# Kernel tuning notes

Measured on AMD Instinct MI355X. Metric: run time of the kernel, lower is better.

The kernel has to match this reference:

```python
import jax, jax.numpy as jnp
import numpy as np

N = 50000   # num_nodes
T = 8       # num_time_steps
C = 64      # feature width (num_features == hidden == num_classes == 64, forced by the module's shape constraints)
E = 800000  # num_edges


def temporal_conv(x, edge_index, time_index, W, b, perturb=None):
    """Faithful TemporalAGNNConv.forward: per-timestep masked scatter-add of
    neighbor features, concat over T, linear + relu. Implemented as a single
    fused (t, dst)-bucketed segment reduce instead of T separate propagates.
    Note: self.lin is dead code in the original; self-loop addition in the
    original would crash (time_index length mismatch) so edges are used as-is.
    """
    src, dst = edge_index[0], edge_index[1]
    msgs = x[src]                                   # [E, C] gather
    seg = time_index * N + dst                      # combined (t, node) bucket
    agg = jax.ops.segment_sum(msgs, seg, num_segments=T * N)   # [T*N, C]
    cat = agg.reshape(T, N, C).transpose(1, 0, 2).reshape(N, T * C)  # [N, T*C]
    out = jax.nn.relu(cat @ W + b)                  # temporal_lin + relu
    if perturb is not None:
        out = out + perturb
    return out


def setup_inputs() -> dict:
    key = jax.random.key(0)
    ks = jax.random.split(key, 11)
    x = jax.random.normal(ks[0], (N, C), jnp.float32)
    edge_index = jax.random.randint(ks[1], (2, E), 0, N, dtype=jnp.int32)
    time_index = jax.random.randint(ks[2], (E,), 0, T, dtype=jnp.int32)
    s_t = 1.0 / np.sqrt(T * C).astype(np.float32)
    # temporal_lin weights stored as [in, out] (torch Linear transposed)
    Wt1 = jax.random.uniform(ks[3], (T * C, C), jnp.float32, -s_t, s_t)
    bt1 = jax.random.uniform(ks[4], (C,), jnp.float32, -s_t, s_t)
    Wt2 = jax.random.uniform(ks[5], (T * C, C), jnp.float32, -s_t, s_t)
    bt2 = jax.random.uniform(ks[6], (C,), jnp.float32, -s_t, s_t)
    s_a1 = 1.0 / np.sqrt(C).astype(np.float32)
    Wa1 = jax.random.uniform(ks[7], (C, 128), jnp.float32, -s_a1, s_a1)
    ba1 = jax.random.uniform(ks[8], (128,), jnp.float32, -s_a1, s_a1)
    s_a2 = 1.0 / np.sqrt(128).astype(np.float32)
    Wa2 = jax.random.uniform(ks[9], (128, C), jnp.float32, -s_a2, s_a2)
    ba2 = jax.random.uniform(ks[10], (C,), jnp.float32, -s_a2, s_a2)
    return {"x": x, "edge_index": edge_index, "time_index": time_index,
            "Wt1": Wt1, "bt1": bt1, "Wt2": Wt2, "bt2": bt2,
            "Wa1": Wa1, "ba1": ba1, "Wa2": Wa2, "ba2": ba2}


def reference(x, edge_index, time_index, Wt1, bt1, Wt2, bt2, Wa1, ba1, Wa2, ba2):
    h1 = jax.nn.relu(temporal_conv(x, edge_index, time_index, Wt1, bt1))   # conv1 + relu
    h2 = temporal_conv(h1, edge_index, time_index, Wt2, bt2)               # conv2 (output width C)
    adv = jax.nn.relu(h2 @ Wa1 + ba1) @ Wa2 + ba2                          # adversary MLP -> [N, C]
    out = temporal_conv(x, edge_index, time_index, Wt1, bt1, perturb=adv)  # conv1 again + perturbation
    return out
```

## Files before the change

### kernel.cpp

```cpp
#include <hip/hip_runtime.h>

#define N_NODES 50000
#define C_FEAT  64
#define E_EDGES 800000
#define KEYS    400000
#define NBLK1   391
#define DPB     16
#define PBLK_X  1563
#define PBLK_W  128
#define PBLK_A  64
#define PBLK_H  3128
#define DPART   6250

typedef __attribute__((ext_vector_type(8))) short short8;
typedef __attribute__((ext_vector_type(4))) float f32x4;

__device__ __forceinline__ float bf2f(unsigned short u) {
    union { unsigned int i; float f; } v; v.i = ((unsigned int)u) << 16; return v.f;
}
__device__ __forceinline__ unsigned short f2bf(float f) {
    union { float f; unsigned int i; } v; v.f = f;
    unsigned int r = v.i + 0x7fff + ((v.i >> 16) & 1);
    return (unsigned short)(r >> 16);
}

__global__ __launch_bounds__(256) void prep_hist(const float* __restrict__ x,
                                                 const float* __restrict__ W1,
                                                 const float* __restrict__ W2,
                                                 const float* __restrict__ Wa1,
                                                 const float* __restrict__ Wa2,
                                                 const int* __restrict__ dst,
                                                 const int* __restrict__ tix,
                                                 unsigned short* __restrict__ xb,
                                                 unsigned short* __restrict__ WT1,
                                                 unsigned short* __restrict__ WT2,
                                                 unsigned short* __restrict__ Wa1T,
                                                 unsigned short* __restrict__ Wa2T,
                                                 int* __restrict__ cnt) {
    const int b = blockIdx.x;
    if (b < PBLK_X) {
        int base = (b * 256 + threadIdx.x) * 8;
        if (base < N_NODES * 64) {
            float4 a = *(const float4*)(x + base);
            float4 c = *(const float4*)(x + base + 4);
            short8 o;
            o[0] = (short)f2bf(a.x); o[1] = (short)f2bf(a.y);
            o[2] = (short)f2bf(a.z); o[3] = (short)f2bf(a.w);
            o[4] = (short)f2bf(c.x); o[5] = (short)f2bf(c.y);
            o[6] = (short)f2bf(c.z); o[7] = (short)f2bf(c.w);
            *(short8*)(xb + base) = o;
        }
    } else if (b < PBLK_X + PBLK_W) {
        int i = (b - PBLK_X) * 256 + threadIdx.x;
        int n = i >> 9, k = i & 511;
        WT1[i] = f2bf(W1[k * 64 + n]);
        WT2[i] = f2bf(W2[k * 64 + n]);
    } else if (b < PBLK_X + PBLK_W + PBLK_A) {
        int i = (b - PBLK_X - PBLK_W) * 256 + threadIdx.x;
        if (i < 8192) {
            int n = i >> 6, k = i & 63;
            Wa1T[i] = f2bf(Wa1[k * 128 + n]);
        } else {
            int ii = i - 8192;
            int n = ii >> 7, k = ii & 127;
            Wa2T[ii] = f2bf(Wa2[k * 64 + n]);
        }
    } else {
        int bb = b - PBLK_X - PBLK_W - PBLK_A;
        const int g = bb & 7;
        const int tile = bb >> 3;
        int e = tile * 2048 + threadIdx.x;
        #pragma unroll
        for (int it = 0; it < 8; ++it, e += 256) {
            if (e < E_EDGES) {
                int d = dst[e];
                if (d / DPART == g)
                    atomicAdd(&cnt[d * 8 + tix[e]], 1);
            }
        }
    }
}

__global__ __launch_bounds__(256) void scan_all(int* __restrict__ cnt,
                                                int* __restrict__ bsum,
                                                int* __restrict__ chunkoff,
                                                int* __restrict__ done) {
    __shared__ int wsum[4];
    __shared__ int ticket;
    const int tid = threadIdx.x;
    const int lane = tid & 63;
    const int wave = tid >> 6;
    const int i4 = blockIdx.x * 256 + tid;
    int4 v = make_int4(0, 0, 0, 0);
    const bool ok = (i4 * 4 < KEYS);
    if (ok) v = ((const int4*)cnt)[i4];
    int s = v.x + v.y + v.z + v.w;
    int sc = s;
    #pragma unroll
    for (int d = 1; d < 64; d <<= 1) {
        int o = __shfl_up(sc, d, 64);
        if (lane >= d) sc += o;
    }
    if (lane == 63) wsum[wave] = sc;
    __syncthreads();
    int wbase = 0;
    #pragma unroll
    for (int w = 0; w < 4; ++w) wbase += (w < wave) ? wsum[w] : 0;
    int base = wbase + sc - s;
    int4 o;
    o.x = base;
    o.y = base + v.x;
    o.z = o.y + v.y;
    o.w = o.z + v.z;
    if (ok) ((int4*)cnt)[i4] = o;
    if (tid == 255) {
        bsum[blockIdx.x] = wbase + sc;
        __threadfence();
        ticket = atomicAdd(done, 1);
    }
    __syncthreads();
    if (ticket == NBLK1 - 1 && wave == 0) {
        int carry = 0;
        #pragma unroll
        for (int g = 0; g < (NBLK1 + 63) / 64; ++g) {
            int j = g * 64 + lane;
            int val = (j < NBLK1) ? atomicAdd(&bsum[j], 0) : 0;
            int scn = val;
            #pragma unroll
            for (int d = 1; d < 64; d <<= 1) {
                int oo = __shfl_up(scn, d, 64);
                if (lane >= d) scn += oo;
            }
            if (j < NBLK1) chunkoff[j] = carry + scn - val;
            carry += __shfl(scn, 63, 64);
        }
    }
}

__global__ __launch_bounds__(256) void scatter_edges(const int* __restrict__ src,
                                                     const int* __restrict__ dst,
                                                     const int* __restrict__ tix,
                                                     int* __restrict__ cursor,
                                                     const int* __restrict__ chunkoff,
                                                     int* __restrict__ elist) {
    const int g = blockIdx.x & 7;
    const int tile = blockIdx.x >> 3;
    int e = tile * 2048 + threadIdx.x;
    #pragma unroll
    for (int it = 0; it < 8; ++it, e += 256) {
        if (e < E_EDGES) {
            int d = dst[e];
            if (d / DPART == g) {
                int t = tix[e];
                int key = d * 8 + t;
                int pos = chunkoff[key >> 10] + atomicAdd(&cursor[key], 1);
                elist[pos] = src[e] | (t << 16);
            }
        }
    }
}

#define FLUSH(T, V)                                                                   \
    { int _t = (T);                                                                   \
      if (_t != cur) { scat[dl][cur * 64 + c] = f2bf(acc); acc = 0.f; cur = _t; }     \
      acc += (V); }

#define EDGE(K)                                                                       \
    int p##K = __builtin_amdgcn_readlane(pv, e + K);                                  \
    float v##K = bf2f(Xb[(size_t)(p##K & 0xffff) * 64 + c]);

__global__ __launch_bounds__(512, 8) void fused_conv(const unsigned short* __restrict__ Xb,
                                                     const unsigned short* __restrict__ WT,
                                                     const float* __restrict__ bias,
                                                     const int* __restrict__ segend,
                                                     const int* __restrict__ chunkoff,
                                                     const int* __restrict__ elist,
                                                     unsigned short* __restrict__ Hb) {
    __shared__ unsigned short scat[DPB][520];
    const int lane = threadIdx.x & 63;
    const int wave = threadIdx.x >> 6;
    const int dbase = blockIdx.x * DPB;
    const int c = lane;

    {
        short8 z = {};
        *(short8*)&scat[wave * 2 + 0][lane * 8] = z;
        *(short8*)&scat[wave * 2 + 1][lane * 8] = z;
    }

    int sbeg[2], send_[2], pvw[2];
    #pragma unroll
    for (int q = 0; q < 2; ++q) {
        const int d = dbase + wave * 2 + q;
        const int k0 = d * 8;
        sbeg[q]  = (d == 0) ? 0 : chunkoff[(k0 - 1) >> 10] + segend[k0 - 1];
        send_[q] = chunkoff[(k0 + 7) >> 10] + segend[k0 + 7];
    }
    #pragma unroll
    for (int q = 0; q < 2; ++q)
        pvw[q] = (lane < send_[q] - sbeg[q]) ? elist[sbeg[q] + lane] : 0;

    #pragma unroll
    for (int q = 0; q < 2; ++q) {
        const int dl = wave * 2 + q;
        int i = sbeg[q];
        const int end = send_[q];
        int pv = pvw[q];
        int cur = 0;
        float acc = 0.f;
        while (i < end) {
            int cnt = end - i; cnt = (cnt > 64) ? 64 : cnt;
            int e = 0;
            for (; e + 7 < cnt; e += 8) {
                EDGE(0) EDGE(1) EDGE(2) EDGE(3) EDGE(4) EDGE(5) EDGE(6) EDGE(7)
                FLUSH(p0 >> 16, v0) FLUSH(p1 >> 16, v1)
                FLUSH(p2 >> 16, v2) FLUSH(p3 >> 16, v3)
                FLUSH(p4 >> 16, v4) FLUSH(p5 >> 16, v5)
                FLUSH(p6 >> 16, v6) FLUSH(p7 >> 16, v7)
            }
            if (e + 3 < cnt) {
                EDGE(0) EDGE(1) EDGE(2) EDGE(3)
                FLUSH(p0 >> 16, v0) FLUSH(p1 >> 16, v1)
                FLUSH(p2 >> 16, v2) FLUSH(p3 >> 16, v3)
                e += 4;
            }
            if (e + 1 < cnt) {
                EDGE(0) EDGE(1)
                FLUSH(p0 >> 16, v0) FLUSH(p1 >> 16, v1)
                e += 2;
            }
            if (e < cnt) {
                EDGE(0)
                FLUSH(p0 >> 16, v0)
            }
            i += 64;
            if (i < end) pv = (lane < end - i) ? elist[i + lane] : 0;
        }
        scat[dl][cur * 64 + c] = f2bf(acc);
    }
    __syncthreads();

    if (wave < 4) {
        const int m = lane & 15;
        const int quad = lane >> 4;
        const int n0 = wave * 16;
        f32x4 acc4 = {0.f, 0.f, 0.f, 0.f};
        const unsigned short* wrow = WT + (size_t)(n0 + m) * 512;
        #pragma unroll
        for (int kc = 0; kc < 16; ++kc) {
            short8 af = *(const short8*)&scat[m][kc * 32 + quad * 8];
            short8 bf = *(const short8*)(wrow + kc * 32 + quad * 8);
            acc4 = __builtin_amdgcn_mfma_f32_16x16x32_bf16(af, bf, acc4, 0, 0, 0);
        }
        const int col = n0 + m;
        const float bcol = bias[col];
        #pragma unroll
        for (int r = 0; r < 4; ++r) {
            int node = dbase + quad * 4 + r;
            Hb[(size_t)node * 64 + col] = f2bf(fmaxf(acc4[r] + bcol, 0.f));
        }
    }
}

__global__ __launch_bounds__(256) void adv_mfma(const unsigned short* __restrict__ h2b,
                                                const unsigned short* __restrict__ Wa1T,
                                                const float* __restrict__ ba1,
                                                const unsigned short* __restrict__ Wa2T,
                                                const float* __restrict__ ba2,
                                                const unsigned short* __restrict__ h1b,
                                                float* __restrict__ out) {
    __shared__ unsigned short sH[64][72];
    __shared__ unsigned short sT[64][136];
    const int nbase = blockIdx.x * 64;
    const int tid = threadIdx.x;
    const int lane = tid & 63;
    const int wave = tid >> 6;
    const int m = lane & 15;
    const int quad = lane >> 4;
    const int r0 = wave * 16;

    #pragma unroll
    for (int i = 0; i < 2; ++i) {
        int idx = tid * 2 + i;
        int row = idx >> 3;
        int c8  = (idx & 7) * 8;
        int node = nbase + row;
        short8 u = {};
        if (node < N_NODES)
            u = *(const short8*)(h2b + (size_t)node * C_FEAT + c8);
        *(short8*)&sH[row][c8] = u;
    }
    __syncthreads();

    {
        f32x4 acc1[8];
        #pragma unroll
        for (int ct = 0; ct < 8; ++ct) acc1[ct] = (f32x4){0.f, 0.f, 0.f, 0.f};
        #pragma unroll
        for (int kc = 0; kc < 2; ++kc) {
            short8 af = *(const short8*)&sH[r0 + m][kc * 32 + quad * 8];
            #pragma unroll
            for (int ct = 0; ct < 8; ++ct) {
                short8 bf = *(const short8*)(Wa1T + (size_t)(ct * 16 + m) * 64 + kc * 32 + quad * 8);
                acc1[ct] = __builtin_amdgcn_mfma_f32_16x16x32_bf16(af, bf, acc1[ct], 0, 0, 0);
            }
        }
        #pragma unroll
        for (int ct = 0; ct < 8; ++ct) {
            const int col = ct * 16 + m;
            const float b1 = ba1[col];
            #pragma unroll
            for (int r = 0; r < 4; ++r)
                sT[r0 + quad * 4 + r][col] = f2bf(fmaxf(acc1[ct][r] + b1, 0.f));
        }
    }
    __syncthreads();

    {
        f32x4 acc2[4];
        #pragma unroll
        for (int ct = 0; ct < 4; ++ct) acc2[ct] = (f32x4){0.f, 0.f, 0.f, 0.f};
        #pragma unroll
        for (int kc = 0; kc < 4; ++kc) {
            short8 af = *(const short8*)&sT[r0 + m][kc * 32 + quad * 8];
            #pragma unroll
            for (int ct = 0; ct < 4; ++ct) {
                short8 bf = *(const short8*)(Wa2T + (size_t)(ct * 16 + m) * 128 + kc * 32 + quad * 8);
                acc2[ct] = __builtin_amdgcn_mfma_f32_16x16x32_bf16(af, bf, acc2[ct], 0, 0, 0);
            }
        }
        #pragma unroll
        for (int ct = 0; ct < 4; ++ct) {
            const int col = ct * 16 + m;
            const float b2 = ba2[col];
            #pragma unroll
            for (int r = 0; r < 4; ++r) {
                int node = nbase + r0 + quad * 4 + r;
                if (node < N_NODES) {
                    float val = acc2[ct][r] + b2 + bf2f(h1b[(size_t)node * 64 + col]);
                    out[(size_t)node * 64 + col] = val;
                }
            }
        }
    }
}

extern "C" void kernel_launch(void* const* d_in, const int* in_sizes, int n_in,
                              void* d_out, int out_size, void* d_ws, size_t ws_size,
                              hipStream_t stream) {
    const float* x   = (const float*)d_in[0];
    const int*   ei  = (const int*)d_in[1];
    const int*   tix = (const int*)d_in[2];
    const float* Wt1 = (const float*)d_in[3];
    const float* bt1 = (const float*)d_in[4];
    const float* Wt2 = (const float*)d_in[5];
    const float* bt2 = (const float*)d_in[6];
    const float* Wa1 = (const float*)d_in[7];
    const float* ba1 = (const float*)d_in[8];
    const float* Wa2 = (const float*)d_in[9];
    const float* ba2 = (const float*)d_in[10];
    float* out = (float*)d_out;

    const int* src = ei;
    const int* dst = ei + E_EDGES;

    unsigned short* xb   = (unsigned short*)d_ws;
    unsigned short* h1b  = xb + (size_t)N_NODES * 64;
    unsigned short* h2b  = h1b + (size_t)N_NODES * 64;
    unsigned short* WT1  = h2b + (size_t)N_NODES * 64;
    unsigned short* WT2  = WT1 + 64 * 512;
    unsigned short* Wa1T = WT2 + 64 * 512;
    unsigned short* Wa2T = Wa1T + 8192;
    int* cnt      = (int*)(Wa2T + 8192);
    int* bsum     = cnt + KEYS;
    int* chunkoff = bsum + 512;
    int* done     = chunkoff + 512;
    int* elist    = done + 64;

    const int cBlk = N_NODES / DPB;
    const int aBlk = (N_NODES + 63) / 64;

    hipMemsetAsync(cnt, 0, (KEYS + 512 + 512 + 64) * sizeof(int), stream);
    prep_hist<<<PBLK_X + PBLK_W + PBLK_A + PBLK_H, 256, 0, stream>>>(
        x, Wt1, Wt2, Wa1, Wa2, dst, tix, xb, WT1, WT2, Wa1T, Wa2T, cnt);
    scan_all<<<NBLK1, 256, 0, stream>>>(cnt, bsum, chunkoff, done);
    scatter_edges<<<8 * 391, 256, 0, stream>>>(src, dst, tix, cnt, chunkoff, elist);

    fused_conv<<<cBlk, 512, 0, stream>>>(xb,  WT1, bt1, cnt, chunkoff, elist, h1b);
    fused_conv<<<cBlk, 512, 0, stream>>>(h1b, WT2, bt2, cnt, chunkoff, elist, h2b);

    adv_mfma<<<aBlk, 256, 0, stream>>>(h2b, Wa1T, ba1, Wa2T, ba2, h1b, out);
}
```

Measured before the change: 290.7 us.

## Balance edge aggregation across waves with LDS float atomics

Fused conv now splits a block's 16-node edge range evenly across its 8 waves instead of giving each wave two fixed nodes. Each lane gathers 4 bf16 features per edge and accumulates with LDS float atomicAdd into an fp32 scratch tile indexed by node and timestep bits packed into the edge word. A zero sentinel row is added to the feature buffers so padded lanes read harmless data. This aims to remove load imbalance from skewed per-node degrees and the serial per-lane flush logic, at the cost of LDS atomic contention and an fp32-to-bf16 conversion before the MFMA.

```diff
diff --git a/kernel.cpp b/kernel.cpp
--- a/kernel.cpp
+++ b/kernel.cpp
@@ -9,11 +9,15 @@
 #define PBLK_X  1563
 #define PBLK_W  128
 #define PBLK_A  64
+#define PBLK_S  1
 #define PBLK_H  3128
 #define DPART   6250
+#define RS      516
+#define SENT    N_NODES
 
 typedef __attribute__((ext_vector_type(8))) short short8;
 typedef __attribute__((ext_vector_type(4))) float f32x4;
+typedef __attribute__((ext_vector_type(4))) unsigned short ushortx4;
 
 __device__ __forceinline__ float bf2f(unsigned short u) {
     union { unsigned int i; float f; } v; v.i = ((unsigned int)u) << 16; return v.f;
@@ -32,6 +36,7 @@
                                                  const int* __restrict__ dst,
                                                  const int* __restrict__ tix,
                                                  unsigned short* __restrict__ xb,
+                                                 unsigned short* __restrict__ h1b,
                                                  unsigned short* __restrict__ WT1,
                                                  unsigned short* __restrict__ WT2,
                                                  unsigned short* __restrict__ Wa1T,
@@ -65,8 +70,12 @@
             int n = ii >> 7, k = ii & 127;
             Wa2T[ii] = f2bf(Wa2[k * 64 + n]);
         }
+    } else if (b < PBLK_X + PBLK_W + PBLK_A + PBLK_S) {
+        int i = threadIdx.x;
+        if (i < 64)       xb[(size_t)N_NODES * 64 + i] = 0;
+        else if (i < 128) h1b[(size_t)N_NODES * 64 + (i - 64)] = 0;
     } else {
-        int bb = b - PBLK_X - PBLK_W - PBLK_A;
+        int bb = b - PBLK_X - PBLK_W - PBLK_A - PBLK_S;
         const int g = bb & 7;
         const int tile = bb >> 3;
         int e = tile * 2048 + threadIdx.x;
@@ -154,20 +163,21 @@
                 int t = tix[e];
                 int key = d * 8 + t;
                 int pos = chunkoff[key >> 10] + atomicAdd(&cursor[key], 1);
-                elist[pos] = src[e] | (t << 16);
-            }
-        }
-    }
-}
-
-#define FLUSH(T, V)                                                                   \
-    { int _t = (T);                                                                   \
-      if (_t != cur) { scat[dl][cur * 64 + c] = f2bf(acc); acc = 0.f; cur = _t; }     \
-      acc += (V); }
-
-#define EDGE(K)                                                                       \
-    int p##K = __builtin_amdgcn_readlane(pv, e + K);                                  \
-    float v##K = bf2f(Xb[(size_t)(p##K & 0xffff) * 64 + c]);
+                elist[pos] = src[e] | (t << 16) | ((d & (DPB - 1)) << 19);
+            }
+        }
+    }
+}
+
+#define BUNDLE(B)                                                                   \
+    {   int p = __shfl(pv, ib + (B), 64);                                           \
+        const unsigned short* px = Xb + ((size_t)(unsigned)(p & 0xffff) << 6) + jb; \
+        ushortx4 u = *(const ushortx4*)px;                                          \
+        float* sp = scatf + ((p >> 19) & 15) * RS + ((p >> 16) & 7) * 64 + jb;      \
+        atomicAdd(sp + 0, bf2f(u[0]));                                              \
+        atomicAdd(sp + 1, bf2f(u[1]));                                              \
+        atomicAdd(sp + 2, bf2f(u[2]));                                              \
+        atomicAdd(sp + 3, bf2f(u[3])); }
 
 __global__ __launch_bounds__(512, 8) void fused_conv(const unsigned short* __restrict__ Xb,
                                                      const unsigned short* __restrict__ WT,
@@ -176,67 +186,34 @@
                                                      const int* __restrict__ chunkoff,
                                                      const int* __restrict__ elist,
                                                      unsigned short* __restrict__ Hb) {
-    __shared__ unsigned short scat[DPB][520];
-    const int lane = threadIdx.x & 63;
-    const int wave = threadIdx.x >> 6;
+    __shared__ __attribute__((aligned(16))) float scatf[DPB * RS];
+    const int tid  = threadIdx.x;
+    const int lane = tid & 63;
+    const int wave = tid >> 6;
     const int dbase = blockIdx.x * DPB;
-    const int c = lane;
-
-    {
-        short8 z = {};
-        *(short8*)&scat[wave * 2 + 0][lane * 8] = z;
-        *(short8*)&scat[wave * 2 + 1][lane * 8] = z;
-    }
-
-    int sbeg[2], send_[2], pvw[2];
-    #pragma unroll
-    for (int q = 0; q < 2; ++q) {
-        const int d = dbase + wave * 2 + q;
-        const int k0 = d * 8;
-        sbeg[q]  = (d == 0) ? 0 : chunkoff[(k0 - 1) >> 10] + segend[k0 - 1];
-        send_[q] = chunkoff[(k0 + 7) >> 10] + segend[k0 + 7];
-    }
-    #pragma unroll
-    for (int q = 0; q < 2; ++q)
-        pvw[q] = (lane < send_[q] - sbeg[q]) ? elist[sbeg[q] + lane] : 0;
-
-    #pragma unroll
-    for (int q = 0; q < 2; ++q) {
-        const int dl = wave * 2 + q;
-        int i = sbeg[q];
-        const int end = send_[q];
-        int pv = pvw[q];
-        int cur = 0;
-        float acc = 0.f;
-        while (i < end) {
-            int cnt = end - i; cnt = (cnt > 64) ? 64 : cnt;
-            int e = 0;
-            for (; e + 7 < cnt; e += 8) {
-                EDGE(0) EDGE(1) EDGE(2) EDGE(3) EDGE(4) EDGE(5) EDGE(6) EDGE(7)
-                FLUSH(p0 >> 16, v0) FLUSH(p1 >> 16, v1)
-                FLUSH(p2 >> 16, v2) FLUSH(p3 >> 16, v3)
-                FLUSH(p4 >> 16, v4) FLUSH(p5 >> 16, v5)
-                FLUSH(p6 >> 16, v6) FLUSH(p7 >> 16, v7)
-            }
-            if (e + 3 < cnt) {
-                EDGE(0) EDGE(1) EDGE(2) EDGE(3)
-                FLUSH(p0 >> 16, v0) FLUSH(p1 >> 16, v1)
-                FLUSH(p2 >> 16, v2) FLUSH(p3 >> 16, v3)
-                e += 4;
-            }
-            if (e + 1 < cnt) {
-                EDGE(0) EDGE(1)
-                FLUSH(p0 >> 16, v0) FLUSH(p1 >> 16, v1)
-                e += 2;
-            }
-            if (e < cnt) {
-                EDGE(0)
-                FLUSH(p0 >> 16, v0)
-            }
-            i += 64;
-            if (i < end) pv = (lane < end - i) ? elist[i + lane] : 0;
-        }
-        scat[dl][cur * 64 + c] = f2bf(acc);
+    const int g  = lane >> 4;
+    const int jb = (lane & 15) << 2;
+
+    for (int i = tid; i < DPB * RS; i += 512) scatf[i] = 0.f;
+
+    const int k0 = dbase * 8;
+    const int beg = (dbase == 0) ? 0 : chunkoff[(k0 - 1) >> 10] + segend[k0 - 1];
+    const int end = chunkoff[(k0 + 127) >> 10] + segend[k0 + 127];
+    const int cntE = end - beg;
+    const int pw = (cntE + 7) >> 3;
+    const int wbeg = beg + wave * pw;
+    int wend = wbeg + pw; if (wend > end) wend = end;
+
+    __syncthreads();
+
+    for (int base = wbeg; base < wend; base += 64) {
+        int nb = wend - base; if (nb > 64) nb = 64;
+        int pv = (lane < nb) ? elist[base + lane] : SENT;
+        const int cpg = (((nb + 3) >> 2) + 3) & ~3;
+        const int ib = g * cpg;
+        for (int b = 0; b < cpg; b += 4) {
+            BUNDLE(b + 0) BUNDLE(b + 1) BUNDLE(b + 2) BUNDLE(b + 3)
+        }
     }
     __syncthreads();
 
@@ -246,9 +223,16 @@
         const int n0 = wave * 16;
         f32x4 acc4 = {0.f, 0.f, 0.f, 0.f};
         const unsigned short* wrow = WT + (size_t)(n0 + m) * 512;
+        const float* arow = scatf + m * RS;
         #pragma unroll
         for (int kc = 0; kc < 16; ++kc) {
-            short8 af = *(const short8*)&scat[m][kc * 32 + quad * 8];
+            f32x4 a0 = *(const f32x4*)(arow + kc * 32 + quad * 8);
+            f32x4 a1 = *(const f32x4*)(arow + kc * 32 + quad * 8 + 4);
+            short8 af;
+            af[0] = (short)f2bf(a0.x); af[1] = (short)f2bf(a0.y);
+            af[2] = (short)f2bf(a0.z); af[3] = (short)f2bf(a0.w);
+            af[4] = (short)f2bf(a1.x); af[5] = (short)f2bf(a1.y);
+            af[6] = (short)f2bf(a1.z); af[7] = (short)f2bf(a1.w);
             short8 bf = *(const short8*)(wrow + kc * 32 + quad * 8);
             acc4 = __builtin_amdgcn_mfma_f32_16x16x32_bf16(af, bf, acc4, 0, 0, 0);
         }
@@ -365,8 +349,8 @@
     const int* dst = ei + E_EDGES;
 
     unsigned short* xb   = (unsigned short*)d_ws;
-    unsigned short* h1b  = xb + (size_t)N_NODES * 64;
-    unsigned short* h2b  = h1b + (size_t)N_NODES * 64;
+    unsigned short* h1b  = xb + (size_t)(N_NODES + 1) * 64;
+    unsigned short* h2b  = h1b + (size_t)(N_NODES + 1) * 64;
     unsigned short* WT1  = h2b + (size_t)N_NODES * 64;
     unsigned short* WT2  = WT1 + 64 * 512;
     unsigned short* Wa1T = WT2 + 64 * 512;
@@ -381,8 +365,8 @@
     const int aBlk = (N_NODES + 63) / 64;
 
     hipMemsetAsync(cnt, 0, (KEYS + 512 + 512 + 64) * sizeof(int), stream);
-    prep_hist<<<PBLK_X + PBLK_W + PBLK_A + PBLK_H, 256, 0, stream>>>(
-        x, Wt1, Wt2, Wa1, Wa2, dst, tix, xb, WT1, WT2, Wa1T, Wa2T, cnt);
+    prep_hist<<<PBLK_X + PBLK_W + PBLK_A + PBLK_S + PBLK_H, 256, 0, stream>>>(
+        x, Wt1, Wt2, Wa1, Wa2, dst, tix, xb, h1b, WT1, WT2, Wa1T, Wa2T, cnt);
     scan_all<<<NBLK1, 256, 0, stream>>>(cnt, bsum, chunkoff, done);
     scatter_edges<<<8 * 391, 256, 0, stream>>>(src, dst, tix, cnt, chunkoff, elist);
 
```

Measured after the change: 911.1 us. 3.13x slower.
